# Optimization experiments

Measured on AMD Instinct MI355X. Metric: run time of the kernel, lower is better.

## Reference

```python
import jax, jax.numpy as jnp
import numpy as np


def setup_inputs() -> dict:
    key = jax.random.key(0)
    k1, k2 = jax.random.split(key)
    B, P, H, W = 224, 12, 512, 512  # bands, endmembers, image rows/cols
    E = jax.random.uniform(k1, (1, B, P), dtype=jnp.float32)
    A = jax.random.uniform(k2, (1, P, H, W), dtype=jnp.float32)
    return {"E": E, "A": A}


def reference(E, A):
    # Fan Model (FM) nonlinear mixing.
    # E: (1, B, P) endmember spectra; A: (1, P, H, W) abundances.
    E0 = E[0]          # (B, P)
    A0 = A[0]          # (P, H, W)
    P = E0.shape[-1]

    # Linear mixing: tensordot(E, A[0], dims=([2],[0])) -> (1, B, H, W)
    linear = jnp.einsum('bp,phw->bhw', E0, A0)

    # Pairwise (i<j) bilinear term, vectorized over all endmember pairs.
    mask = jnp.triu(jnp.ones((P, P), dtype=E0.dtype), k=1)        # strict upper triangle
    pairE = (E0[:, :, None] * E0[:, None, :]) * mask               # (B, P, P)
    pairA = A0[:, None, :, :] * A0[None, :, :, :]                  # (P, P, H, W)
    nonlinear = jnp.einsum('bij,ijhw->bhw', pairE, pairA)          # (B, H, W)

    return (linear + nonlinear)[None]  # (1, B, H, W)
```

## Files before the change

### kernel.cpp

```cpp
#include <hip/hip_runtime.h>


#define NP 12
#define NB 224
#define HW (512 * 512)
#define BPG 28
#define NGRP 8
#define BLOCK 256

typedef float vfloat4 __attribute__((ext_vector_type(4)));

__global__ __launch_bounds__(BLOCK) void fan_mix(const float* __restrict__ E,
                                                 const float* __restrict__ A,
                                                 float* __restrict__ out) {
    const int x4 = blockIdx.x * BLOCK + threadIdx.x;
    const int b0 = blockIdx.y * BPG;

    const vfloat4* __restrict__ A4 = (const vfloat4*)A;
    vfloat4* __restrict__ O4 = (vfloat4*)out;

    vfloat4 a[NP];
#pragma unroll
    for (int p = 0; p < NP; ++p) {
        a[p] = A4[(size_t)p * (HW / 4) + x4];
    }

#pragma unroll 4
    for (int b = b0; b < b0 + BPG; ++b) {
        vfloat4 L = 0.f, Q = 0.f;
#pragma unroll
        for (int p = 0; p < NP; ++p) {
            float e = E[b * NP + p];
            vfloat4 t = e * a[p];
            L += t;
            Q += t * t;
        }
        vfloat4 r = L + 0.5f * (L * L - Q);
        O4[(size_t)b * (HW / 4) + x4] = r;
    }
}

extern "C" void kernel_launch(void* const* d_in, const int* in_sizes, int n_in,
                              void* d_out, int out_size, void* d_ws, size_t ws_size,
                              hipStream_t stream) {
    const float* E = (const float*)d_in[0];
    const float* A = (const float*)d_in[1];
    float* out = (float*)d_out;

    dim3 grid(HW / (4 * BLOCK), NGRP);
    fan_mix<<<grid, BLOCK, 0, stream>>>(E, A, out);
}
```

Baseline: 244.0 us.

## Process two pixel quads per thread and remap blocks across XCDs

Each thread now handles two float4 pixel groups, which halves the grid in x and reuses each scalar E load for twice as much arithmetic. Block indices are also permuted so that consecutive logical tiles are spread across the 8 XCDs, with the aim of improving locality or balance of A reads across band groups. The costs are doubled register use for the abundance arrays, which may reduce occupancy, and fewer blocks in flight. The kernel is write-bandwidth bound, so the gain is likely small.

```diff
diff --git a/kernel.cpp b/kernel.cpp
--- a/kernel.cpp
+++ b/kernel.cpp
@@ -4,39 +4,51 @@
 #define NP 12
 #define NB 224
 #define HW (512 * 512)
+#define NQ (HW / 4)
 #define BPG 28
 #define NGRP 8
 #define BLOCK 256
+#define PQ 2
+#define QPB (BLOCK * PQ)
+#define GX (NQ / QPB)
+#define NXCD 8
 
 typedef float vfloat4 __attribute__((ext_vector_type(4)));
 
 __global__ __launch_bounds__(BLOCK) void fan_mix(const float* __restrict__ E,
                                                  const float* __restrict__ A,
                                                  float* __restrict__ out) {
-    const int x4 = blockIdx.x * BLOCK + threadIdx.x;
+    const int gx = blockIdx.x;
+    const int lx = (gx % NXCD) * (GX / NXCD) + gx / NXCD;
+    const int q0 = lx * QPB + threadIdx.x;
     const int b0 = blockIdx.y * BPG;
 
     const vfloat4* __restrict__ A4 = (const vfloat4*)A;
     vfloat4* __restrict__ O4 = (vfloat4*)out;
 
-    vfloat4 a[NP];
+    vfloat4 a0[NP], a1[NP];
 #pragma unroll
     for (int p = 0; p < NP; ++p) {
-        a[p] = A4[(size_t)p * (HW / 4) + x4];
+        a0[p] = A4[(size_t)p * NQ + q0];
+        a1[p] = A4[(size_t)p * NQ + q0 + BLOCK];
     }
 
-#pragma unroll 4
+#pragma unroll 2
     for (int b = b0; b < b0 + BPG; ++b) {
-        vfloat4 L = 0.f, Q = 0.f;
+        vfloat4 L0 = 0.f, Q0 = 0.f, L1 = 0.f, Q1 = 0.f;
 #pragma unroll
         for (int p = 0; p < NP; ++p) {
             float e = E[b * NP + p];
-            vfloat4 t = e * a[p];
-            L += t;
-            Q += t * t;
+            vfloat4 t0 = e * a0[p];
+            vfloat4 t1 = e * a1[p];
+            L0 += t0;  Q0 += t0 * t0;
+            L1 += t1;  Q1 += t1 * t1;
         }
-        vfloat4 r = L + 0.5f * (L * L - Q);
-        O4[(size_t)b * (HW / 4) + x4] = r;
+        vfloat4 r0 = L0 + 0.5f * (L0 * L0 - Q0);
+        vfloat4 r1 = L1 + 0.5f * (L1 * L1 - Q1);
+        const size_t o = (size_t)b * NQ + q0;
+        O4[o] = r0;
+        O4[o + BLOCK] = r1;
     }
 }
 
@@ -47,6 +59,6 @@
     const float* A = (const float*)d_in[1];
     float* out = (float*)d_out;
 
-    dim3 grid(HW / (4 * BLOCK), NGRP);
+    dim3 grid(GX, NGRP);
     fan_mix<<<grid, BLOCK, 0, stream>>>(E, A, out);
 }
```

Result: no change. 241.4 us (-1.1%).
